# Kernel tuning notes

Hardware: AMD Instinct MI355X
Metric: run time of the kernel (lower is better)

## Reference

```python
import jax, jax.numpy as jnp
import numpy as np
from math import sqrt

FACTOR = 5

def setup_inputs() -> dict:
    key = jax.random.key(0)
    kq, kk, kv, ka = jax.random.split(key, 4)
    B, L, H, D = 4, 2048, 8, 64
    return {
        "queries": jax.random.normal(kq, (B, L, H, D), dtype=jnp.float32),
        "keys": jax.random.normal(kk, (B, L, H, D), dtype=jnp.float32),
        "values": jax.random.normal(kv, (B, L, H, D), dtype=jnp.float32),
        "atten_data": jax.random.normal(ka, (B, L, 2), dtype=jnp.float32),
        "attn_mask": jnp.zeros((1,), dtype=bool),  # unused (mask_flag=False)
    }

def reference(queries, keys, values, atten_data, attn_mask):
    # layer_num=1, mask_flag=False, output_attention=False, scale=None
    B, L_Q, H, D = queries.shape
    L_K = keys.shape[1]
    U_part = min(FACTOR * int(np.ceil(np.log(L_K))), L_K)  # sample_k
    u = min(FACTOR * int(np.ceil(np.log(L_Q))), L_Q)       # n_top

    Q = jnp.transpose(queries, (0, 2, 1, 3))  # [B,H,L_Q,D]
    K = jnp.transpose(keys, (0, 2, 1, 3))     # [B,H,L_K,D]
    V = jnp.transpose(values, (0, 2, 1, 3))   # [B,H,L_V,D]

    # --- _prob_QK: random K sampling per query position ---
    index_sample = jax.random.randint(jax.random.key(42), (L_Q, U_part), 0, L_K)
    K_sample = K[:, :, index_sample, :]                      # [B,H,L_Q,U_part,D]
    Q_K_sample = jnp.einsum("bhld,bhlsd->bhls", Q, K_sample)  # [B,H,L_Q,U_part]
    M = Q_K_sample.max(axis=-1) - Q_K_sample.sum(axis=-1) / L_K  # [B,H,L_Q]
    _, M_top = jax.lax.top_k(M, u)                           # [B,H,u]

    Q_reduce = jnp.take_along_axis(Q, M_top[..., None], axis=2)  # [B,H,u,D]
    scores_top = jnp.einsum("bhud,bhkd->bhuk", Q_reduce, K)      # [B,H,u,L_K]

    scale = 1.0 / sqrt(D)
    scores_top = scores_top * scale

    # --- initial context: mean of V broadcast over L_Q (mask_flag=False) ---
    V_mean = V.mean(axis=-2, keepdims=True)                  # [B,H,1,D]
    context = jnp.broadcast_to(V_mean, (B, H, L_Q, D))

    # --- update context at top-u query positions ---
    attn = jax.nn.softmax(scores_top, axis=-1)               # [B,H,u,L_K]
    upd = jnp.einsum("bhuk,bhkd->bhud", attn, V)             # [B,H,u,D]
    bidx = jnp.arange(B)[:, None, None]
    hidx = jnp.arange(H)[None, :, None]
    context = context.at[bidx, hidx, M_top].set(upd)

    return jnp.transpose(context, (0, 2, 1, 3))  # [B,L_Q,H,D]
```

## Files before the change

kernel.cpp:

```cpp
#include <hip/hip_runtime.h>
#include <math.h>

#define B_  4
#define L_  2048
#define H_  8
#define D_  64
#define U_  40
#define HD  (H_*D_)

#define WS_NEED_KC16 5600256

struct U2 { unsigned a, b; };

__host__ __device__ constexpr unsigned rotl32c(unsigned x, int r){
  return (x<<r)|(x>>(32-r));
}

__host__ __device__ constexpr U2 tf2x32(unsigned k0, unsigned k1,
                                        unsigned x0, unsigned x1)
{
  const unsigned k2 = k0 ^ k1 ^ 0x1BD11BDAu;
  const int rA[4] = {13,15,26,6};
  const int rB[4] = {17,29,16,24};
  x0 += k0; x1 += k1;
  for (int i=0;i<4;i++){ x0+=x1; x1=rotl32c(x1,rA[i]); x1^=x0; }
  x0 += k1; x1 += k2 + 1u;
  for (int i=0;i<4;i++){ x0+=x1; x1=rotl32c(x1,rB[i]); x1^=x0; }
  x0 += k2; x1 += k0 + 2u;
  for (int i=0;i<4;i++){ x0+=x1; x1=rotl32c(x1,rA[i]); x1^=x0; }
  x0 += k0; x1 += k1 + 3u;
  for (int i=0;i<4;i++){ x0+=x1; x1=rotl32c(x1,rB[i]); x1^=x0; }
  x0 += k1; x1 += k2 + 4u;
  for (int i=0;i<4;i++){ x0+=x1; x1=rotl32c(x1,rA[i]); x1^=x0; }
  x0 += k2; x1 += k0 + 5u;
  return U2{x0, x1};
}

__global__ __launch_bounds__(256) void mvm_kernel(const float* __restrict__ q,
                                                  const float* __restrict__ k,
                                                  const float* __restrict__ v,
                                                  float* __restrict__ M,
                                                  float* __restrict__ vmean)
{
  __shared__ float red[2][2][8][2];
  int tid = threadIdx.x;
  int w = tid >> 6, lane = tid & 63;

  if (blockIdx.x < 512){
    int g = blockIdx.x;
    int bh = g & 31, chunk = g >> 5;
    int b = bh >> 3, h = bh & 7;
    int l0 = chunk*128 + w*32;
    float s = 0.f;
    for (int i=0;i<32;i++)
      s += v[(size_t)(b*L_ + l0 + i)*HD + h*D_ + lane];
    atomicAdd(&vmean[bh*D_ + lane], s);
    return;
  }

  int g     = blockIdx.x - 512;
  int b     = g & 3;
  int lpair = g >> 2;
  int ll    = w >> 1;
  int half  = w & 1;
  int l     = lpair*2 + ll;
  int h     = lane >> 3, d8 = lane & 7;

  const float* qrow = q + (size_t)(b*L_ + l)*HD;
  float4 q0 = *(const float4*)(qrow + lane*8);
  float4 q1 = *(const float4*)(qrow + lane*8 + 4);

  constexpr U2 K2 = tf2x32(0u, 42u, 0u, 1u);
  int myidx = 0;
  if (lane < U_){
    U2 r = tf2x32(K2.a, K2.b, 0u, (unsigned)(l*U_ + lane));
    myidx = (int)((r.a ^ r.b) & 2047u);
  }

  const float* kb = k + (size_t)b*L_*HD;
  float vmax = -INFINITY, vsum = 0.f;
  #pragma unroll 10
  for (int s=0;s<20;s++){
    int kidx = __shfl(myidx, half*20 + s, 64);
    const float* kr = kb + (size_t)kidx*HD;
    float4 k0 = *(const float4*)(kr + lane*8);
    float4 k1 = *(const float4*)(kr + lane*8 + 4);
    float p = q0.x*k0.x + q0.y*k0.y + q0.z*k0.z + q0.w*k0.w
            + q1.x*k1.x + q1.y*k1.y + q1.z*k1.z + q1.w*k1.w;
    p += __shfl_xor(p, 1, 64);
    p += __shfl_xor(p, 2, 64);
    p += __shfl_xor(p, 4, 64);
    vmax = fmaxf(vmax, p);
    vsum += p;
  }
  if (d8 == 0){ red[ll][half][h][0] = vmax; red[ll][half][h][1] = vsum; }
  __syncthreads();
  if (half == 0 && d8 == 0){
    float m2 = red[ll][1][h][0], s2 = red[ll][1][h][1];
    float fm = fmaxf(vmax, m2);
    float fs = vsum + s2;
    M[(b*8 + h)*L_ + l] = fm - fs * (1.0f/(float)L_);
  }
}

__global__ __launch_bounds__(256) void topk_init_kernel(const float* __restrict__ M,
                                                        const float* __restrict__ vmean,
                                                        int*   __restrict__ mtop,
                                                        float* __restrict__ out)
{
  int tid = threadIdx.x;

  if (blockIdx.x >= 32){
    int i = (blockIdx.x - 32)*256 + tid;
    int d4 = i & 15;
    int h  = (i >> 4) & 7;
    int bl = i >> 7;
    int b  = bl >> 11;
    float4 vm = ((const float4*)(vmean + (b*H_ + h)*D_))[d4];
    const float sc = 1.0f/(float)L_;
    float4 o; o.x = vm.x*sc; o.y = vm.y*sc; o.z = vm.z*sc; o.w = vm.w*sc;
    ((float4*)out)[i] = o;
    return;
  }

  __shared__ unsigned keys[L_];
  __shared__ unsigned hist[256];
  __shared__ unsigned sh_prefix, sh_need, sh_cgt, sh_ceq;
  int bh = blockIdx.x;

  #pragma unroll
  for (int i=0;i<8;i++){
    unsigned bits = __float_as_uint(M[bh*L_ + tid + 256*i]);
    keys[tid + 256*i] = (bits & 0x80000000u) ? ~bits : (bits | 0x80000000u);
  }
  if (tid == 0){ sh_prefix = 0u; sh_need = U_; sh_cgt = 0u; sh_ceq = 0u; }

  unsigned pmask = 0u;
  for (int p = 3; p >= 0; --p){
    hist[tid] = 0u;
    __syncthreads();
    unsigned pref = sh_prefix;
    #pragma unroll
    for (int i=0;i<8;i++){
      unsigned key = keys[tid + 256*i];
      if ((key & pmask) == pref)
        atomicAdd(&hist[(key >> (8*p)) & 255u], 1u);
    }
    __syncthreads();

    if (tid < 64){
      unsigned h0 = hist[tid*4+0], h1 = hist[tid*4+1];
      unsigned h2 = hist[tid*4+2], h3 = hist[tid*4+3];
      unsigned loc = h0+h1+h2+h3;
      unsigned s = loc;
      #pragma unroll
      for (int off=1; off<64; off<<=1){
        unsigned o = __shfl_down(s, off, 64);
        if (tid + off < 64) s += o;
      }
      unsigned need = sh_need;
      unsigned cum = s - loc;
      unsigned bsel = 0xFFFFFFFFu, nn = 0u;
      if (cum < need && cum + h3 >= need){ bsel = tid*4+3; nn = need - cum; }
      cum += h3;
      if (bsel==0xFFFFFFFFu && cum < need && cum + h2 >= need){ bsel = tid*4+2; nn = need - cum; }
      cum += h2;
      if (bsel==0xFFFFFFFFu && cum < need && cum + h1 >= need){ bsel = tid*4+1; nn = need - cum; }
      cum += h1;
      if (bsel==0xFFFFFFFFu && cum < need && cum + h0 >= need){ bsel = tid*4+0; nn = need - cum; }
      if (bsel != 0xFFFFFFFFu){
        sh_prefix = sh_prefix | (bsel << (8*p));
        sh_need = nn;
      }
    }
    __syncthreads();
    pmask |= 0xFFu << (8*p);
  }

  unsigned K40 = sh_prefix;
  unsigned need = sh_need;
  #pragma unroll
  for (int i=0;i<8;i++){
    int idx = tid + 256*i;
    unsigned key = keys[idx];
    if (key > K40){
      unsigned pos = atomicAdd(&sh_cgt, 1u);
      mtop[bh*U_ + pos] = idx;
    } else if (key == K40){
      unsigned e = atomicAdd(&sh_ceq, 1u);
      if (e < need) mtop[bh*U_ + (U_ - need) + e] = idx;
    }
  }
}

__global__ __launch_bounds__(512, 4) void attn_kernel(const float* __restrict__ q,
                                                      const float* __restrict__ k,
                                                      const float* __restrict__ v,
                                                      const int*   __restrict__ mtop,
                                                      float* __restrict__ pacc,
                                                      float* __restrict__ pl,
                                                      int nt, int KC)
{
  __shared__ float sh[128*68 + 128*64 + 40*64];
  float* Kt  = sh;
  float* Vt  = sh + 128*68;
  float* Qs  = sh + 128*68 + 128*64;
  float* psQ = sh;

  int g  = blockIdx.x;
  int bh = g & 31, kc = g >> 5;
  int b = bh >> 3, h = bh & 7;
  int tid = threadIdx.x, w = tid >> 6, lane = tid & 63;

  #pragma unroll
  for (int c=0;c<2;c++){
    int flat = c*512 + tid;
    if (flat < 640){
      int row = flat >> 4, col = flat & 15;
      int lstar = mtop[bh*U_ + row];
      ((float4*)(Qs + row*64))[col] =
        ((const float4*)(q + (size_t)(b*L_ + lstar)*HD + h*D_))[col];
    }
  }

  float acc[5], lsum[5];
  #pragma unroll
  for (int qq=0;qq<5;qq++){ acc[qq] = 0.f; lsum[qq] = 0.f; }

  for (int tt=0; tt<nt; ++tt){
    int kt = (kc*nt + tt)*128;
    if (tt) __syncthreads();
    #pragma unroll
    for (int c=0;c<4;c++){
      int flat = c*512 + tid;
      int row = flat >> 4, col = flat & 15;
      ((float4*)(Kt + row*68))[col] =
        ((const float4*)(k + (size_t)(b*L_ + kt + row)*HD + h*D_))[col];
      ((float4*)(Vt + row*64))[col] =
        ((const float4*)(v + (size_t)(b*L_ + kt + row)*HD + h*D_))[col];
    }
    __syncthreads();

    float s0[5], s1[5];
    #pragma unroll
    for (int qq=0;qq<5;qq++){ s0[qq] = 0.f; s1[qq] = 0.f; }
    const float* kr0 = Kt + lane*68;
    const float* kr1 = Kt + (lane+64)*68;
    #pragma unroll
    for (int t=0;t<16;t++){
      float4 k0 = ((const float4*)kr0)[t];
      float4 k1 = ((const float4*)kr1)[t];
      #pragma unroll
      for (int qq=0;qq<5;qq++){
        float4 qf = ((const float4*)(Qs + (w*5+qq)*64))[t];
        s0[qq] += k0.x*qf.x + k0.y*qf.y + k0.z*qf.z + k0.w*qf.w;
        s1[qq] += k1.x*qf.x + k1.y*qf.y + k1.z*qf.z + k1.w*qf.w;
      }
    }
    __syncthreads();

    #pragma unroll
    for (int qq=0;qq<5;qq++){
      float p0 = __expf(s0[qq]*0.125f);
      float p1 = __expf(s1[qq]*0.125f);
      psQ[(w*5+qq)*128 + lane]      = p0;
      psQ[(w*5+qq)*128 + lane + 64] = p1;
      lsum[qq] += p0 + p1;
    }

    #pragma unroll 4
    for (int k4=0;k4<32;k4++){
      float v0 = Vt[(4*k4+0)*64 + lane];
      float v1 = Vt[(4*k4+1)*64 + lane];
      float v2 = Vt[(4*k4+2)*64 + lane];
      float v3 = Vt[(4*k4+3)*64 + lane];
      #pragma unroll
      for (int qq=0;qq<5;qq++){
        float4 pp = ((const float4*)(psQ + (w*5+qq)*128))[k4];
        acc[qq] += pp.x*v0 + pp.y*v1 + pp.z*v2 + pp.w*v3;
      }
    }
  }

  #pragma unroll
  for (int qq=0;qq<5;qq++){
    float ls = lsum[qq];
    #pragma unroll
    for (int off=32; off; off>>=1) ls += __shfl_xor(ls, off, 64);
    int gu = bh*U_ + w*5 + qq;
    pacc[(size_t)(gu*KC + kc)*64 + lane] = acc[qq];
    if (lane == 0) pl[gu*KC + kc] = ls;
  }
}

__global__ __launch_bounds__(256) void combine_kernel(const int* __restrict__ mtop,
                                                      const float* __restrict__ pacc,
                                                      const float* __restrict__ pl,
                                                      float* __restrict__ out,
                                                      int KC)
{
  int gu = blockIdx.x*4 + (threadIdx.x >> 6);
  int lane = threadIdx.x & 63;
  int bh = gu / U_, u = gu - bh*U_;
  float a = 0.f, L = 0.f;
  for (int c=0;c<KC;c++){
    a += pacc[(size_t)(gu*KC + c)*64 + lane];
    L += pl[gu*KC + c];
  }
  int b = bh >> 3, h = bh & 7;
  int lstar = mtop[bh*U_ + u];
  out[(size_t)(b*L_ + lstar)*HD + h*D_ + lane] = a / L;
}

extern "C" void kernel_launch(void* const* d_in, const int* in_sizes, int n_in,
                              void* d_out, int out_size, void* d_ws, size_t ws_size,
                              hipStream_t stream)
{
  const float* q = (const float*)d_in[0];
  const float* k = (const float*)d_in[1];
  const float* v = (const float*)d_in[2];
  float* out = (float*)d_out;

  int KC = (ws_size >= (size_t)WS_NEED_KC16) ? 16 : 8;
  int nt = 16 / KC;

  size_t o_pl    = (size_t)1280*KC*64*4;
  size_t o_vmean = o_pl + (size_t)1280*KC*4;
  size_t o_M     = o_vmean + 2048*4;
  size_t o_mtop  = o_M + 65536*4;

  float* pacc  = (float*)d_ws;
  float* pl    = (float*)((char*)d_ws + o_pl);
  float* vmean = (float*)((char*)d_ws + o_vmean);
  float* M     = (float*)((char*)d_ws + o_M);
  int*   mtop  = (int*)  ((char*)d_ws + o_mtop);

  hipMemsetAsync(vmean, 0, 2048*sizeof(float), stream);
  mvm_kernel      <<<4608,  256, 0, stream>>>(q, k, v, M, vmean);
  topk_init_kernel<<<4128,  256, 0, stream>>>(M, vmean, mtop, out);
  attn_kernel     <<<32*KC, 512, 0, stream>>>(q, k, v, mtop, pacc, pl, nt, KC);
  combine_kernel  <<<320,   256, 0, stream>>>(mtop, pacc, pl, out, KC);
}
```

Before: 168.2 us.

## Split attention into smaller query-group blocks and batch sampled K loads

The attention kernel now uses 256-thread blocks, each handling 20 of the 40 selected queries against 64-row K/V tiles. The key dimension is split into up to 32 chunks, giving more blocks for better occupancy and parallelism at the cost of more partial results for the combine step. The sampling kernel precomputes all shuffled indices and issues 10 gathered K-row loads back to back before computing, to expose memory-level parallelism. It also gains a launch-bounds occupancy hint.

```diff
diff --git a/kernel.cpp b/kernel.cpp
--- a/kernel.cpp
+++ b/kernel.cpp
@@ -8,7 +8,7 @@
 #define U_  40
 #define HD  (H_*D_)
 
-#define WS_NEED_KC16 5600256
+#define WS_NEED_KC32 21410816
 
 struct U2 { unsigned a, b; };
 
@@ -36,11 +36,11 @@
   return U2{x0, x1};
 }
 
-__global__ __launch_bounds__(256) void mvm_kernel(const float* __restrict__ q,
-                                                  const float* __restrict__ k,
-                                                  const float* __restrict__ v,
-                                                  float* __restrict__ M,
-                                                  float* __restrict__ vmean)
+__global__ __launch_bounds__(256, 4) void mvm_kernel(const float* __restrict__ q,
+                                                     const float* __restrict__ k,
+                                                     const float* __restrict__ v,
+                                                     float* __restrict__ M,
+                                                     float* __restrict__ vmean)
 {
   __shared__ float red[2][2][8][2];
   int tid = threadIdx.x;
@@ -77,21 +77,31 @@
     myidx = (int)((r.a ^ r.b) & 2047u);
   }
 
+  int kidx[20];
+  #pragma unroll
+  for (int s=0;s<20;s++) kidx[s] = __shfl(myidx, half*20 + s, 64);
+
   const float* kb = k + (size_t)b*L_*HD;
   float vmax = -INFINITY, vsum = 0.f;
-  #pragma unroll 10
-  for (int s=0;s<20;s++){
-    int kidx = __shfl(myidx, half*20 + s, 64);
-    const float* kr = kb + (size_t)kidx*HD;
-    float4 k0 = *(const float4*)(kr + lane*8);
-    float4 k1 = *(const float4*)(kr + lane*8 + 4);
-    float p = q0.x*k0.x + q0.y*k0.y + q0.z*k0.z + q0.w*k0.w
-            + q1.x*k1.x + q1.y*k1.y + q1.z*k1.z + q1.w*k1.w;
-    p += __shfl_xor(p, 1, 64);
-    p += __shfl_xor(p, 2, 64);
-    p += __shfl_xor(p, 4, 64);
-    vmax = fmaxf(vmax, p);
-    vsum += p;
+  #pragma unroll
+  for (int batch=0; batch<2; ++batch){
+    float4 ka[10], kc2[10];
+    #pragma unroll
+    for (int j=0;j<10;j++){
+      const float* kr = kb + (size_t)kidx[batch*10+j]*HD;
+      ka[j]  = *(const float4*)(kr + lane*8);
+      kc2[j] = *(const float4*)(kr + lane*8 + 4);
+    }
+    #pragma unroll
+    for (int j=0;j<10;j++){
+      float p = q0.x*ka[j].x + q0.y*ka[j].y + q0.z*ka[j].z + q0.w*ka[j].w
+              + q1.x*kc2[j].x + q1.y*kc2[j].y + q1.z*kc2[j].z + q1.w*kc2[j].w;
+      p += __shfl_xor(p, 1, 64);
+      p += __shfl_xor(p, 2, 64);
+      p += __shfl_xor(p, 4, 64);
+      vmax = fmaxf(vmax, p);
+      vsum += p;
+    }
   }
   if (d8 == 0){ red[ll][half][h][0] = vmax; red[ll][half][h][1] = vsum; }
   __syncthreads();
@@ -193,7 +203,7 @@
   }
 }
 
-__global__ __launch_bounds__(512, 4) void attn_kernel(const float* __restrict__ q,
+__global__ __launch_bounds__(256, 4) void attn_kernel(const float* __restrict__ q,
                                                       const float* __restrict__ k,
                                                       const float* __restrict__ v,
                                                       const int*   __restrict__ mtop,
@@ -201,23 +211,24 @@
                                                       float* __restrict__ pl,
                                                       int nt, int KC)
 {
-  __shared__ float sh[128*68 + 128*64 + 40*64];
+  __shared__ float sh[64*68 + 64*64 + 20*64];
   float* Kt  = sh;
-  float* Vt  = sh + 128*68;
-  float* Qs  = sh + 128*68 + 128*64;
+  float* Vt  = sh + 64*68;
+  float* Qs  = sh + 64*68 + 64*64;
   float* psQ = sh;
 
   int g  = blockIdx.x;
-  int bh = g & 31, kc = g >> 5;
+  int bh = g & 31, j = g >> 5;
+  int kc = j >> 1, qg = j & 1;
   int b = bh >> 3, h = bh & 7;
   int tid = threadIdx.x, w = tid >> 6, lane = tid & 63;
 
   #pragma unroll
   for (int c=0;c<2;c++){
-    int flat = c*512 + tid;
-    if (flat < 640){
+    int flat = c*256 + tid;
+    if (flat < 320){
       int row = flat >> 4, col = flat & 15;
-      int lstar = mtop[bh*U_ + row];
+      int lstar = mtop[bh*U_ + qg*20 + row];
       ((float4*)(Qs + row*64))[col] =
         ((const float4*)(q + (size_t)(b*L_ + lstar)*HD + h*D_))[col];
     }
@@ -228,11 +239,11 @@
   for (int qq=0;qq<5;qq++){ acc[qq] = 0.f; lsum[qq] = 0.f; }
 
   for (int tt=0; tt<nt; ++tt){
-    int kt = (kc*nt + tt)*128;
+    int kt = (kc*nt + tt)*64;
     if (tt) __syncthreads();
     #pragma unroll
     for (int c=0;c<4;c++){
-      int flat = c*512 + tid;
+      int flat = c*256 + tid;
       int row = flat >> 4, col = flat & 15;
       ((float4*)(Kt + row*68))[col] =
         ((const float4*)(k + (size_t)(b*L_ + kt + row)*HD + h*D_))[col];
@@ -241,20 +252,17 @@
     }
     __syncthreads();
 
-    float s0[5], s1[5];
-    #pragma unroll
-    for (int qq=0;qq<5;qq++){ s0[qq] = 0.f; s1[qq] = 0.f; }
+    float s0[5];
+    #pragma unroll
+    for (int qq=0;qq<5;qq++) s0[qq] = 0.f;
     const float* kr0 = Kt + lane*68;
-    const float* kr1 = Kt + (lane+64)*68;
     #pragma unroll
     for (int t=0;t<16;t++){
       float4 k0 = ((const float4*)kr0)[t];
-      float4 k1 = ((const float4*)kr1)[t];
       #pragma unroll
       for (int qq=0;qq<5;qq++){
         float4 qf = ((const float4*)(Qs + (w*5+qq)*64))[t];
         s0[qq] += k0.x*qf.x + k0.y*qf.y + k0.z*qf.z + k0.w*qf.w;
-        s1[qq] += k1.x*qf.x + k1.y*qf.y + k1.z*qf.z + k1.w*qf.w;
       }
     }
     __syncthreads();
@@ -262,21 +270,19 @@
     #pragma unroll
     for (int qq=0;qq<5;qq++){
       float p0 = __expf(s0[qq]*0.125f);
-      float p1 = __expf(s1[qq]*0.125f);
-      psQ[(w*5+qq)*128 + lane]      = p0;
-      psQ[(w*5+qq)*128 + lane + 64] = p1;
-      lsum[qq] += p0 + p1;
+      psQ[(w*5+qq)*64 + lane] = p0;
+      lsum[qq] += p0;
     }
 
     #pragma unroll 4
-    for (int k4=0;k4<32;k4++){
+    for (int k4=0;k4<16;k4++){
       float v0 = Vt[(4*k4+0)*64 + lane];
       float v1 = Vt[(4*k4+1)*64 + lane];
       float v2 = Vt[(4*k4+2)*64 + lane];
       float v3 = Vt[(4*k4+3)*64 + lane];
       #pragma unroll
       for (int qq=0;qq<5;qq++){
-        float4 pp = ((const float4*)(psQ + (w*5+qq)*128))[k4];
+        float4 pp = ((const float4*)(psQ + (w*5+qq)*64))[k4];
         acc[qq] += pp.x*v0 + pp.y*v1 + pp.z*v2 + pp.w*v3;
       }
     }
@@ -287,7 +293,7 @@
     float ls = lsum[qq];
     #pragma unroll
     for (int off=32; off; off>>=1) ls += __shfl_xor(ls, off, 64);
-    int gu = bh*U_ + w*5 + qq;
+    int gu = bh*U_ + qg*20 + w*5 + qq;
     pacc[(size_t)(gu*KC + kc)*64 + lane] = acc[qq];
     if (lane == 0) pl[gu*KC + kc] = ls;
   }
@@ -321,8 +327,8 @@
   const float* v = (const float*)d_in[2];
   float* out = (float*)d_out;
 
-  int KC = (ws_size >= (size_t)WS_NEED_KC16) ? 16 : 8;
-  int nt = 16 / KC;
+  int KC = (ws_size >= (size_t)WS_NEED_KC32) ? 32 : 16;
+  int nt = 32 / KC;
 
   size_t o_pl    = (size_t)1280*KC*64*4;
   size_t o_vmean = o_pl + (size_t)1280*KC*4;
@@ -338,6 +344,6 @@
   hipMemsetAsync(vmean, 0, 2048*sizeof(float), stream);
   mvm_kernel      <<<4608,  256, 0, stream>>>(q, k, v, M, vmean);
   topk_init_kernel<<<4128,  256, 0, stream>>>(M, vmean, mtop, out);
-  attn_kernel     <<<32*KC, 512, 0, stream>>>(q, k, v, mtop, pacc, pl, nt, KC);
+  attn_kernel     <<<64*KC, 256, 0, stream>>>(q, k, v, mtop, pacc, pl, nt, KC);
   combine_kernel  <<<320,   256, 0, stream>>>(mtop, pacc, pl, out, KC);
 }
```

After: 170.5 us. No clear change (+1.4%).

## Split attn blocks by query half and register-prefetch next K/V tile

Applied to the files above, without the earlier changes.

The attention kernel now uses 256-thread blocks that each handle half of the 40 selected queries, so there are twice as many blocks per key chunk. Key chunks become larger (KC 8 instead of 16, two tiles per block). The next K/V tile is prefetched into registers while the current tile is processed, which overlaps global loads with compute. The probability buffer gets its own shared region and is processed in two 64-key halves, which removes one barrier per tile. In exchange, register pressure rises from the 16 float4 prefetch registers, and each block reloads K/V for only half as many queries, doubling K/V traffic per key.

```diff
diff --git a/kernel.cpp b/kernel.cpp
--- a/kernel.cpp
+++ b/kernel.cpp
@@ -8,7 +8,7 @@
 #define U_  40
 #define HD  (H_*D_)
 
-#define WS_NEED_KC16 5600256
+#define WS_NEED_KC8 2937856
 
 struct U2 { unsigned a, b; };
 
@@ -193,7 +193,7 @@
   }
 }
 
-__global__ __launch_bounds__(512, 4) void attn_kernel(const float* __restrict__ q,
+__global__ __launch_bounds__(256, 2) void attn_kernel(const float* __restrict__ q,
                                                       const float* __restrict__ k,
                                                       const float* __restrict__ v,
                                                       const int*   __restrict__ mtop,
@@ -201,46 +201,57 @@
                                                       float* __restrict__ pl,
                                                       int nt, int KC)
 {
-  __shared__ float sh[128*68 + 128*64 + 40*64];
+  __shared__ float sh[128*68 + 128*64 + 20*64 + 20*64];
   float* Kt  = sh;
   float* Vt  = sh + 128*68;
   float* Qs  = sh + 128*68 + 128*64;
-  float* psQ = sh;
+  float* psQ = Qs + 20*64;
 
   int g  = blockIdx.x;
-  int bh = g & 31, kc = g >> 5;
+  int bh = g & 31, j = g >> 5;
+  int kc = j >> 1, qg = j & 1;
   int b = bh >> 3, h = bh & 7;
   int tid = threadIdx.x, w = tid >> 6, lane = tid & 63;
 
-  #pragma unroll
-  for (int c=0;c<2;c++){
-    int flat = c*512 + tid;
-    if (flat < 640){
-      int row = flat >> 4, col = flat & 15;
-      int lstar = mtop[bh*U_ + row];
-      ((float4*)(Qs + row*64))[col] =
-        ((const float4*)(q + (size_t)(b*L_ + lstar)*HD + h*D_))[col];
-    }
-  }
+  int srow = (w<<5) + (lane>>4);
+  int scol = lane & 15;
+
+  float4 kreg[8], vreg[8];
+  {
+    int kt0 = (kc*nt)*128;
+    const float4* kg = (const float4*)(k + (size_t)(b*L_ + kt0 + srow)*HD + h*D_) + scol;
+    const float4* vg = (const float4*)(v + (size_t)(b*L_ + kt0 + srow)*HD + h*D_) + scol;
+    #pragma unroll
+    for (int i=0;i<8;i++){ kreg[i] = kg[i*512]; vreg[i] = vg[i*512]; }
+  }
+
+  {
+    int r0 = lane >> 4, c = lane & 15;
+    int row = w*5 + r0;
+    int lstar = mtop[bh*U_ + qg*20 + row];
+    ((float4*)(Qs + row*64))[c] =
+      ((const float4*)(q + (size_t)(b*L_ + lstar)*HD + h*D_))[c];
+    if (lane < 16){
+      int row4 = w*5 + 4;
+      int l4 = mtop[bh*U_ + qg*20 + row4];
+      ((float4*)(Qs + row4*64))[c] =
+        ((const float4*)(q + (size_t)(b*L_ + l4)*HD + h*D_))[c];
+    }
+  }
+
+  #pragma unroll
+  for (int i=0;i<8;i++){
+    int row = (w<<5) + (i<<2) + (lane>>4);
+    ((float4*)(Kt + row*68))[scol] = kreg[i];
+    ((float4*)(Vt + (row<<6)))[scol] = vreg[i];
+  }
+  __syncthreads();
 
   float acc[5], lsum[5];
   #pragma unroll
   for (int qq=0;qq<5;qq++){ acc[qq] = 0.f; lsum[qq] = 0.f; }
 
   for (int tt=0; tt<nt; ++tt){
-    int kt = (kc*nt + tt)*128;
-    if (tt) __syncthreads();
-    #pragma unroll
-    for (int c=0;c<4;c++){
-      int flat = c*512 + tid;
-      int row = flat >> 4, col = flat & 15;
-      ((float4*)(Kt + row*68))[col] =
-        ((const float4*)(k + (size_t)(b*L_ + kt + row)*HD + h*D_))[col];
-      ((float4*)(Vt + row*64))[col] =
-        ((const float4*)(v + (size_t)(b*L_ + kt + row)*HD + h*D_))[col];
-    }
-    __syncthreads();
-
     float s0[5], s1[5];
     #pragma unroll
     for (int qq=0;qq<5;qq++){ s0[qq] = 0.f; s1[qq] = 0.f; }
@@ -257,28 +268,48 @@
         s1[qq] += k1.x*qf.x + k1.y*qf.y + k1.z*qf.z + k1.w*qf.w;
       }
     }
+
+    if (tt+1 < nt){
+      int kt1 = (kc*nt + tt + 1)*128;
+      const float4* kg = (const float4*)(k + (size_t)(b*L_ + kt1 + srow)*HD + h*D_) + scol;
+      const float4* vg = (const float4*)(v + (size_t)(b*L_ + kt1 + srow)*HD + h*D_) + scol;
+      #pragma unroll
+      for (int i=0;i<8;i++){ kreg[i] = kg[i*512]; vreg[i] = vg[i*512]; }
+    }
+
+    #pragma unroll
+    for (int half=0; half<2; ++half){
+      #pragma unroll
+      for (int qq=0;qq<5;qq++){
+        float p = __expf((half ? s1[qq] : s0[qq])*0.125f);
+        psQ[(w*5+qq)*64 + lane] = p;
+        lsum[qq] += p;
+      }
+      #pragma unroll 4
+      for (int k4=0;k4<16;k4++){
+        int rb = half*64 + k4*4;
+        float v0 = Vt[(rb+0)*64 + lane];
+        float v1 = Vt[(rb+1)*64 + lane];
+        float v2 = Vt[(rb+2)*64 + lane];
+        float v3 = Vt[(rb+3)*64 + lane];
+        #pragma unroll
+        for (int qq=0;qq<5;qq++){
+          float4 pp = ((const float4*)(psQ + (w*5+qq)*64))[k4];
+          acc[qq] += pp.x*v0 + pp.y*v1 + pp.z*v2 + pp.w*v3;
+        }
+      }
+    }
+
     __syncthreads();
 
-    #pragma unroll
-    for (int qq=0;qq<5;qq++){
-      float p0 = __expf(s0[qq]*0.125f);
-      float p1 = __expf(s1[qq]*0.125f);
-      psQ[(w*5+qq)*128 + lane]      = p0;
-      psQ[(w*5+qq)*128 + lane + 64] = p1;
-      lsum[qq] += p0 + p1;
-    }
-
-    #pragma unroll 4
-    for (int k4=0;k4<32;k4++){
-      float v0 = Vt[(4*k4+0)*64 + lane];
-      float v1 = Vt[(4*k4+1)*64 + lane];
-      float v2 = Vt[(4*k4+2)*64 + lane];
-      float v3 = Vt[(4*k4+3)*64 + lane];
-      #pragma unroll
-      for (int qq=0;qq<5;qq++){
-        float4 pp = ((const float4*)(psQ + (w*5+qq)*128))[k4];
-        acc[qq] += pp.x*v0 + pp.y*v1 + pp.z*v2 + pp.w*v3;
-      }
+    if (tt+1 < nt){
+      #pragma unroll
+      for (int i=0;i<8;i++){
+        int row = (w<<5) + (i<<2) + (lane>>4);
+        ((float4*)(Kt + row*68))[scol] = kreg[i];
+        ((float4*)(Vt + (row<<6)))[scol] = vreg[i];
+      }
+      __syncthreads();
     }
   }
 
@@ -287,7 +318,7 @@
     float ls = lsum[qq];
     #pragma unroll
     for (int off=32; off; off>>=1) ls += __shfl_xor(ls, off, 64);
-    int gu = bh*U_ + w*5 + qq;
+    int gu = bh*U_ + qg*20 + w*5 + qq;
     pacc[(size_t)(gu*KC + kc)*64 + lane] = acc[qq];
     if (lane == 0) pl[gu*KC + kc] = ls;
   }
@@ -321,7 +352,7 @@
   const float* v = (const float*)d_in[2];
   float* out = (float*)d_out;
 
-  int KC = (ws_size >= (size_t)WS_NEED_KC16) ? 16 : 8;
+  int KC = (ws_size >= (size_t)WS_NEED_KC8) ? 8 : 4;
   int nt = 16 / KC;
 
   size_t o_pl    = (size_t)1280*KC*64*4;
@@ -338,6 +369,6 @@
   hipMemsetAsync(vmean, 0, 2048*sizeof(float), stream);
   mvm_kernel      <<<4608,  256, 0, stream>>>(q, k, v, M, vmean);
   topk_init_kernel<<<4128,  256, 0, stream>>>(M, vmean, mtop, out);
-  attn_kernel     <<<32*KC, 512, 0, stream>>>(q, k, v, mtop, pacc, pl, nt, KC);
+  attn_kernel     <<<64*KC, 256, 0, stream>>>(q, k, v, mtop, pacc, pl, nt, KC);
   combine_kernel  <<<320,   256, 0, stream>>>(mtop, pacc, pl, out, KC);
 }
```

After: 304.0 us. 80.7% more time.
